# Kernel optimization log

Hardware: AMD Instinct MI355X
Metric: run time of the kernel (lower is better)

## Reference

```python
import jax, jax.numpy as jnp
import numpy as np

EPS = 1e-6
TEMPERATURE = 0.75
SINKHORN_ITERS = 7
BUCKETS = 128


def setup_inputs() -> dict:
    key = jax.random.key(0)
    k1, k2, k3, k4, k5 = jax.random.split(key, 5)
    b, h, t, dh = 2, 8, 8192, 128
    q = jax.random.normal(k1, (b, h, t, dh), dtype=jnp.float32)
    k = jax.random.normal(k2, (b, h, t, dh), dtype=jnp.float32)
    v = jax.random.normal(k3, (b, h, t, dh), dtype=jnp.float32)
    # SimpleSortNet linear: (1, heads, 2*dim_head, buckets)
    W_sort = jax.random.normal(k4, (1, h, 2 * dh, BUCKETS), dtype=jnp.float32)
    # uniform noise used to build gumbel samples (torch samples internally)
    u_gumbel = jax.random.uniform(k5, (b * h, BUCKETS, BUCKETS), dtype=jnp.float32)
    return {"q": q, "k": k, "v": v, "W_sort": W_sort, "u_gumbel": u_gumbel}


def _gumbel_sinkhorn(R, u):
    # R >= 0 (post-relu). r = (log(R+eps) + gumbel) / temperature
    g = -jnp.log(-jnp.log(u + EPS) + EPS)
    r = (jnp.log(R + EPS) + g) / TEMPERATURE
    for _ in range(SINKHORN_ITERS):
        r = r - jax.nn.logsumexp(r, axis=2, keepdims=True)
        r = r - jax.nn.logsumexp(r, axis=1, keepdims=True)
    return jnp.exp(r)


def reference(q, k, v, W_sort, u_gumbel):
    b, h, t, dh = q.shape
    dim = h * dh  # full model dim, used for the softmax scale (matches torch)
    bh = b * h
    buckets = W_sort.shape[-1]
    bsz = t // buckets

    qm = q.reshape(bh, t, dh)
    km = k.reshape(bh, t, dh)
    vm = v.reshape(bh, t, dh)

    b_q = qm.reshape(bh, buckets, bsz, dh)
    b_k = km.reshape(bh, buckets, bsz, dh)
    b_v = vm.reshape(bh, buckets, bsz, dh)

    # SimpleSortNet: per-bucket sums of q and k -> linear -> relu
    x = jnp.concatenate([b_q.sum(axis=2), b_k.sum(axis=2)], axis=-1)  # (bh, buckets, 2*dh)
    W = jnp.broadcast_to(W_sort, (b, h, 2 * dh, buckets)).reshape(bh, 2 * dh, buckets)
    R = jax.nn.relu(jnp.einsum('bue,bek->buk', x, W))  # (bh, buckets, buckets)

    R = _gumbel_sinkhorn(R, u_gumbel)

    # zero_all_but_top along dim=2 with k=1 (keep argmax entry per row)
    idx = jnp.argmax(R, axis=2, keepdims=True)  # (bh, buckets, 1)
    mask = jnp.arange(buckets)[None, None, :] == idx
    R = jnp.where(mask, R, 0.0)

    # reorder buckets: butd = sum_v R[buv] * b_k[bvtd]
    b_k_r = jnp.einsum('buv,bvtd->butd', R, b_k)
    b_v_r = jnp.einsum('buv,bvtd->butd', R, b_v)

    b_k_cat = jnp.concatenate([b_k_r, b_k], axis=2)  # (bh, buckets, 2*bsz, dh)
    b_v_cat = jnp.concatenate([b_v_r, b_v], axis=2)

    dots = jnp.einsum('buie,buje->buij', b_q, b_k_cat) * (dim ** -0.5)
    attn = jax.nn.softmax(dots, axis=-1)
    out = jnp.einsum('buij,buje->buie', attn, b_v_cat)  # (bh, buckets, bsz, dh)

    return out.reshape(b, h, t, dh)
```

## Files before the change

kernel.cpp:

```cpp
#include <hip/hip_runtime.h>
#include <hip/hip_bf16.h>

#define T_SEQ   8192
#define DH      128
#define NBH     16
#define NBUCK   128
#define BSZ     64
#define EPSF    1e-6f

#define SWZ(r) (((((r) & 7) ^ (((r) >> 3) & 7))) << 3)

typedef __attribute__((ext_vector_type(8))) __bf16 bf16x8;
typedef __attribute__((ext_vector_type(4))) float  f32x4;

static __device__ __forceinline__ unsigned short f2bf(float f) {
  __bf16 h = (__bf16)f;
  return __builtin_bit_cast(unsigned short, h);
}

__global__ __launch_bounds__(256) void k_bsum(
    const float* __restrict__ q, const float* __restrict__ k,
    float* __restrict__ x) {
  const int u = blockIdx.x, bh = blockIdx.y, which = blockIdx.z;
  const int t = threadIdx.x;
  const int c4g = t & 31;
  const int r0  = (t >> 5) << 3;
  const float* src = which ? k : q;
  const float* p = src + ((size_t)bh * T_SEQ + (size_t)u * BSZ + r0) * DH + c4g * 4;
  float4 acc = {0.f, 0.f, 0.f, 0.f};
  #pragma unroll
  for (int r = 0; r < 8; r++) {
    float4 vv = *(const float4*)(p + (size_t)r * DH);
    acc.x += vv.x; acc.y += vv.y; acc.z += vv.z; acc.w += vv.w;
  }
  __shared__ float4 xr[8][32];
  xr[t >> 5][c4g] = acc;
  __syncthreads();
  if (t < 32) {
    float4 s4 = xr[0][t];
    #pragma unroll
    for (int j = 1; j < 8; j++) {
      float4 o = xr[j][t];
      s4.x += o.x; s4.y += o.y; s4.z += o.z; s4.w += o.w;
    }
    *(float4*)(x + ((size_t)bh * NBUCK + u) * 256 + which * 128 + t * 4) = s4;
  }
}

__global__ __launch_bounds__(128) void k_sortgemm(
    const float* __restrict__ x, const float* __restrict__ W,
    const float* __restrict__ ug, float* __restrict__ rbuf) {
  const int u0 = blockIdx.x * 4, bh = blockIdx.y;
  const int v = threadIdx.x;
  __shared__ float xs[4][256];
  for (int i = v; i < 1024; i += 128)
    xs[i >> 8][i & 255] = x[((size_t)bh * NBUCK + u0 + (i >> 8)) * 256 + (i & 255)];
  __syncthreads();
  const float* Wp = W + (size_t)(bh & 7) * 256 * NBUCK + v;
  float acc0 = 0.f, acc1 = 0.f, acc2 = 0.f, acc3 = 0.f;
  #pragma unroll 16
  for (int e = 0; e < 256; e++) {
    float we = Wp[(size_t)e * NBUCK];
    acc0 += xs[0][e] * we;
    acc1 += xs[1][e] * we;
    acc2 += xs[2][e] * we;
    acc3 += xs[3][e] * we;
  }
  float accs[4] = {acc0, acc1, acc2, acc3};
  #pragma unroll
  for (int j = 0; j < 4; j++) {
    float R = fmaxf(accs[j], 0.f) + EPSF;
    float gu = ug[((size_t)bh * NBUCK + u0 + j) * NBUCK + v] + EPSF;
    float g = -logf(-logf(gu) + EPSF);
    rbuf[((size_t)bh * NBUCK + u0 + j) * NBUCK + v] = (logf(R) + g) * (1.f / 0.75f);
  }
}

__global__ __launch_bounds__(512, 1) void k_sinkhorn(
    const float* __restrict__ rbuf, int* __restrict__ idxb, float* __restrict__ sb) {
  const int bh = blockIdx.x;
  const int t  = threadIdx.x;
  const int own = t >> 2;
  const int qq  = t & 3;
  __shared__ float rl[128 * 129];
  __shared__ float ca[128], ra[128];

  const float* rb = rbuf + (size_t)bh * (NBUCK * NBUCK);
  for (int i = t; i < NBUCK * NBUCK; i += 512)
    rl[(i >> 7) * 129 + (i & 127)] = rb[i];
  if (t < 128) ca[t] = 0.f;
  __syncthreads();

  float rowv[32], colv[32];
  #pragma unroll
  for (int i4 = 0; i4 < 8; i4++) {
    float4 vv = *(const float4*)(&rl[own * 129 + qq * 32 + i4 * 4]);
    rowv[i4 * 4 + 0] = vv.x; rowv[i4 * 4 + 1] = vv.y;
    rowv[i4 * 4 + 2] = vv.z; rowv[i4 * 4 + 3] = vv.w;
  }
  #pragma unroll
  for (int i = 0; i < 32; i++) colv[i] = rl[(qq * 32 + i) * 129 + own];

  for (int iter = 0; iter < 7; iter++) {
    {
      float vals[32];
      float m = -1e30f;
      #pragma unroll
      for (int i4 = 0; i4 < 8; i4++) {
        float4 cc = *(const float4*)(&ca[qq * 32 + i4 * 4]);
        vals[i4 * 4 + 0] = rowv[i4 * 4 + 0] + cc.x;
        vals[i4 * 4 + 1] = rowv[i4 * 4 + 1] + cc.y;
        vals[i4 * 4 + 2] = rowv[i4 * 4 + 2] + cc.z;
        vals[i4 * 4 + 3] = rowv[i4 * 4 + 3] + cc.w;
      }
      #pragma unroll
      for (int i = 0; i < 32; i++) m = fmaxf(m, vals[i]);
      m = fmaxf(m, __shfl_xor(m, 1));
      m = fmaxf(m, __shfl_xor(m, 2));
      float s0 = 0.f, s1 = 0.f, s2 = 0.f, s3 = 0.f;
      #pragma unroll
      for (int i = 0; i < 8; i++) {
        s0 += __expf(vals[i * 4 + 0] - m);
        s1 += __expf(vals[i * 4 + 1] - m);
        s2 += __expf(vals[i * 4 + 2] - m);
        s3 += __expf(vals[i * 4 + 3] - m);
      }
      float ss = (s0 + s1) + (s2 + s3);
      ss += __shfl_xor(ss, 1);
      ss += __shfl_xor(ss, 2);
      if (qq == 0) ra[own] = -(m + logf(ss));
    }
    __syncthreads();
    {
      float vals[32];
      float m = -1e30f;
      #pragma unroll
      for (int i4 = 0; i4 < 8; i4++) {
        float4 rr = *(const float4*)(&ra[qq * 32 + i4 * 4]);
        vals[i4 * 4 + 0] = colv[i4 * 4 + 0] + rr.x;
        vals[i4 * 4 + 1] = colv[i4 * 4 + 1] + rr.y;
        vals[i4 * 4 + 2] = colv[i4 * 4 + 2] + rr.z;
        vals[i4 * 4 + 3] = colv[i4 * 4 + 3] + rr.w;
      }
      #pragma unroll
      for (int i = 0; i < 32; i++) m = fmaxf(m, vals[i]);
      m = fmaxf(m, __shfl_xor(m, 1));
      m = fmaxf(m, __shfl_xor(m, 2));
      float s0 = 0.f, s1 = 0.f, s2 = 0.f, s3 = 0.f;
      #pragma unroll
      for (int i = 0; i < 8; i++) {
        s0 += __expf(vals[i * 4 + 0] - m);
        s1 += __expf(vals[i * 4 + 1] - m);
        s2 += __expf(vals[i * 4 + 2] - m);
        s3 += __expf(vals[i * 4 + 3] - m);
      }
      float ss = (s0 + s1) + (s2 + s3);
      ss += __shfl_xor(ss, 1);
      ss += __shfl_xor(ss, 2);
      if (qq == 0) ca[own] = -(m + logf(ss));
    }
    __syncthreads();
  }

  {
    float best = -1e30f; int bi = qq * 32;
    #pragma unroll
    for (int i = 0; i < 32; i++) {
      float val = rowv[i] + ca[qq * 32 + i];
      if (val > best) { best = val; bi = qq * 32 + i; }
    }
    #pragma unroll
    for (int d = 1; d < 4; d <<= 1) {
      float ob = __shfl_xor(best, d);
      int   oi = __shfl_xor(bi, d);
      if (ob > best || (ob == best && oi < bi)) { best = ob; bi = oi; }
    }
    if (qq == 0) {
      idxb[bh * NBUCK + own] = bi;
      sb[bh * NBUCK + own]   = expf(rl[own * 129 + bi] + ra[own] + ca[bi]);
    }
  }
}

__global__ __launch_bounds__(256) void k_attn(
    const float* __restrict__ q, const float* __restrict__ k, const float* __restrict__ v,
    const int* __restrict__ idxb, const float* __restrict__ sb, float* __restrict__ out) {
  const int u  = blockIdx.x;
  const int bh = blockIdx.y;
  const int t  = threadIdx.x;
  const int lane = t & 63;
  const int w  = t >> 6;
  const int l15 = lane & 15;
  const int lgp = lane >> 4;

  __shared__ uint4 smem4[2048];
  unsigned short* sm = (unsigned short*)smem4;
  #define VOFF 8192

  const int   vidx = idxb[bh * NBUCK + u];
  const float sval = sb[bh * NBUCK + u];
  const size_t hb = (size_t)bh * (T_SEQ * DH);
  const float* qg = q + hb;
  const float* kg = k + hb;
  const float* vg = v + hb;

  #pragma unroll
  for (int it = 0; it < 16; it++) {
    int i = it * 256 + t;
    int row = i >> 5;
    int c4 = (i & 31) << 2;
    int grow = (row < 64) ? (vidx * BSZ + row) : (u * BSZ + (row - 64));
    float4 val = *(const float4*)(kg + (size_t)grow * DH + c4);
    ushort4 hh;
    hh.x = f2bf(val.x); hh.y = f2bf(val.y); hh.z = f2bf(val.z); hh.w = f2bf(val.w);
    *(ushort4*)(sm + (((row * 128 + c4) ^ SWZ(row)))) = hh;
  }
  bf16x8 aQ[4];
  {
    int qrow = u * BSZ + w * 16 + l15;
    const float* qp = qg + (size_t)qrow * DH + lgp * 8;
    #pragma unroll
    for (int kk = 0; kk < 4; kk++) {
      float4 v0 = *(const float4*)(qp + kk * 32);
      float4 v1 = *(const float4*)(qp + kk * 32 + 4);
      bf16x8 f;
      f[0] = (__bf16)v0.x; f[1] = (__bf16)v0.y; f[2] = (__bf16)v0.z; f[3] = (__bf16)v0.w;
      f[4] = (__bf16)v1.x; f[5] = (__bf16)v1.y; f[6] = (__bf16)v1.z; f[7] = (__bf16)v1.w;
      aQ[kk] = f;
    }
  }
  float4 vpre1[8];
  #pragma unroll
  for (int it = 0; it < 8; it++) {
    int i = it * 256 + t;
    int d0 = (i & 31) << 2;
    int j  = i >> 5;
    vpre1[it] = *(const float4*)(vg + (size_t)(vidx * BSZ + j) * DH + d0);
  }
  __syncthreads();

  f32x4 accS[8];
  __builtin_amdgcn_s_setprio(1);
  #pragma unroll
  for (int n = 0; n < 8; n++) {
    f32x4 acc = {0.f, 0.f, 0.f, 0.f};
    #pragma unroll
    for (int kk = 0; kk < 4; kk++) {
      int row = n * 16 + l15;
      int c0 = lgp * 8 + kk * 32;
      bf16x8 bK = *(const bf16x8*)(sm + ((row * 128 + c0) ^ SWZ(row)));
      acc = __builtin_amdgcn_mfma_f32_16x16x32_bf16(aQ[kk], bK, acc, 0, 0, 0);
    }
    accS[n] = acc;
  }
  __builtin_amdgcn_s_setprio(0);

  float pval[8][4];
  float lsum[4];
  #pragma unroll
  for (int r = 0; r < 4; r++) {
    float mm = -1e30f;
    #pragma unroll
    for (int n = 0; n < 8; n++) {
      float lg2 = accS[n][r] * 0.03125f * (n < 4 ? sval : 1.0f);
      pval[n][r] = lg2;
      mm = fmaxf(mm, lg2);
    }
    mm = fmaxf(mm, __shfl_xor(mm, 1));
    mm = fmaxf(mm, __shfl_xor(mm, 2));
    mm = fmaxf(mm, __shfl_xor(mm, 4));
    mm = fmaxf(mm, __shfl_xor(mm, 8));
    float ss = 0.f;
    #pragma unroll
    for (int n = 0; n < 8; n++) {
      float p = __expf(pval[n][r] - mm);
      ss += p;
      pval[n][r] = p * (n < 4 ? sval : 1.0f);
    }
    ss += __shfl_xor(ss, 1);
    ss += __shfl_xor(ss, 2);
    ss += __shfl_xor(ss, 4);
    ss += __shfl_xor(ss, 8);
    lsum[r] = ss;
  }

  __syncthreads();

  #pragma unroll
  for (int n = 0; n < 8; n++) {
    #pragma unroll
    for (int r = 0; r < 4; r++) {
      int prow = w * 16 + lgp * 4 + r;
      int pcol = n * 16 + l15;
      sm[(prow * 128 + pcol) ^ SWZ(prow)] = f2bf(pval[n][r]);
    }
  }
  #pragma unroll
  for (int it = 0; it < 8; it++) {
    int i = it * 256 + t;
    int d0 = (i & 31) << 2;
    int j  = i >> 5;
    float4 val = vpre1[it];
    sm[VOFF + (((d0 + 0) * 64 + j) ^ SWZ(d0 + 0))] = f2bf(val.x);
    sm[VOFF + (((d0 + 1) * 64 + j) ^ SWZ(d0 + 1))] = f2bf(val.y);
    sm[VOFF + (((d0 + 2) * 64 + j) ^ SWZ(d0 + 2))] = f2bf(val.z);
    sm[VOFF + (((d0 + 3) * 64 + j) ^ SWZ(d0 + 3))] = f2bf(val.w);
  }
  float4 vpre2[8];
  #pragma unroll
  for (int it = 0; it < 8; it++) {
    int i = it * 256 + t;
    int d0 = (i & 31) << 2;
    int j  = i >> 5;
    vpre2[it] = *(const float4*)(vg + (size_t)(u * BSZ + j) * DH + d0);
  }
  __syncthreads();

  bf16x8 aP[4];
  #pragma unroll
  for (int kk = 0; kk < 4; kk++) {
    int prow = w * 16 + l15;
    int c0 = lgp * 8 + kk * 32;
    aP[kk] = *(const bf16x8*)(sm + ((prow * 128 + c0) ^ SWZ(prow)));
  }

  f32x4 accO[8];
  __builtin_amdgcn_s_setprio(1);
  #pragma unroll
  for (int n = 0; n < 8; n++) {
    f32x4 acc = {0.f, 0.f, 0.f, 0.f};
    #pragma unroll
    for (int kk = 0; kk < 2; kk++) {
      int d = n * 16 + l15;
      int jj0 = lgp * 8 + kk * 32;
      bf16x8 bV = *(const bf16x8*)(sm + VOFF + ((d * 64 + jj0) ^ SWZ(d)));
      acc = __builtin_amdgcn_mfma_f32_16x16x32_bf16(aP[kk], bV, acc, 0, 0, 0);
    }
    accO[n] = acc;
  }
  __builtin_amdgcn_s_setprio(0);
  __syncthreads();

  #pragma unroll
  for (int it = 0; it < 8; it++) {
    int i = it * 256 + t;
    int d0 = (i & 31) << 2;
    int j  = i >> 5;
    float4 val = vpre2[it];
    sm[VOFF + (((d0 + 0) * 64 + j) ^ SWZ(d0 + 0))] = f2bf(val.x);
    sm[VOFF + (((d0 + 1) * 64 + j) ^ SWZ(d0 + 1))] = f2bf(val.y);
    sm[VOFF + (((d0 + 2) * 64 + j) ^ SWZ(d0 + 2))] = f2bf(val.z);
    sm[VOFF + (((d0 + 3) * 64 + j) ^ SWZ(d0 + 3))] = f2bf(val.w);
  }
  __syncthreads();

  float invl[4];
  #pragma unroll
  for (int r = 0; r < 4; r++) invl[r] = 1.0f / lsum[r];

  __builtin_amdgcn_s_setprio(1);
  #pragma unroll
  for (int n = 0; n < 8; n++) {
    f32x4 acc = accO[n];
    #pragma unroll
    for (int kk = 2; kk < 4; kk++) {
      int d = n * 16 + l15;
      int jj0 = lgp * 8 + (kk - 2) * 32;
      bf16x8 bV = *(const bf16x8*)(sm + VOFF + ((d * 64 + jj0) ^ SWZ(d)));
      acc = __builtin_amdgcn_mfma_f32_16x16x32_bf16(aP[kk], bV, acc, 0, 0, 0);
    }
    #pragma unroll
    for (int r = 0; r < 4; r++) {
      int i2 = w * 16 + lgp * 4 + r;
      int d = n * 16 + l15;
      out[((size_t)bh * T_SEQ + (size_t)u * BSZ + i2) * DH + d] = acc[r] * invl[r];
    }
  }
  __builtin_amdgcn_s_setprio(0);
}

extern "C" void kernel_launch(void* const* d_in, const int* in_sizes, int n_in,
                              void* d_out, int out_size, void* d_ws, size_t ws_size,
                              hipStream_t stream) {
  (void)in_sizes; (void)n_in; (void)out_size; (void)ws_size;
  const float* q  = (const float*)d_in[0];
  const float* k  = (const float*)d_in[1];
  const float* v  = (const float*)d_in[2];
  const float* W  = (const float*)d_in[3];
  const float* ug = (const float*)d_in[4];
  float* out = (float*)d_out;

  float* xbuf = (float*)d_ws;
  float* rbuf = xbuf + (size_t)NBH * NBUCK * 256;
  int*   idxb = (int*)(rbuf + (size_t)NBH * NBUCK * NBUCK);
  float* sb   = (float*)(idxb + NBH * NBUCK);

  k_bsum    <<<dim3(NBUCK, NBH, 2), 256, 0, stream>>>(q, k, xbuf);
  k_sortgemm<<<dim3(32, NBH),       128, 0, stream>>>(xbuf, W, ug, rbuf);
  k_sinkhorn<<<NBH,                 512, 0, stream>>>(rbuf, idxb, sb);
  k_attn    <<<dim3(NBUCK, NBH),    256, 0, stream>>>(q, k, v, idxb, sb, out);
}
```

Measured before the change: 114.0 us.

## Read K fragments directly from global and stage full V transposed in LDS

The attention kernel no longer stages K in shared memory. Each wave loads its K MFMA operand fragments straight from global memory and converts them to bf16 in registers. The LDS instead holds the full 128-row V tile transposed, filled in one pass, plus a separate P region, so the PV product runs as a single 4-step MFMA loop and several barriers and the split V staging go away. The trade-off is K rows being re-read from global/L2 by all four waves, more LDS per block, and scattered 2-byte LDS stores for the V transpose.

```diff
diff --git a/kernel.cpp b/kernel.cpp
--- a/kernel.cpp
+++ b/kernel.cpp
@@ -193,9 +193,9 @@
   const int l15 = lane & 15;
   const int lgp = lane >> 4;
 
-  __shared__ uint4 smem4[2048];
+  __shared__ uint4 smem4[3072];
   unsigned short* sm = (unsigned short*)smem4;
-  #define VOFF 8192
+  #define PB 16384
 
   const int   vidx = idxb[bh * NBUCK + u];
   const float sval = sb[bh * NBUCK + u];
@@ -207,14 +207,16 @@
   #pragma unroll
   for (int it = 0; it < 16; it++) {
     int i = it * 256 + t;
-    int row = i >> 5;
-    int c4 = (i & 31) << 2;
-    int grow = (row < 64) ? (vidx * BSZ + row) : (u * BSZ + (row - 64));
-    float4 val = *(const float4*)(kg + (size_t)grow * DH + c4);
-    ushort4 hh;
-    hh.x = f2bf(val.x); hh.y = f2bf(val.y); hh.z = f2bf(val.z); hh.w = f2bf(val.w);
-    *(ushort4*)(sm + (((row * 128 + c4) ^ SWZ(row)))) = hh;
-  }
+    int j = i & 127;
+    int d0 = (i >> 7) << 2;
+    int grow = (j < 64) ? (vidx * BSZ + j) : (u * BSZ + (j - 64));
+    float4 val = *(const float4*)(vg + (size_t)grow * DH + d0);
+    sm[(((d0 + 0) * 128 + j) ^ SWZ(d0 + 0))] = f2bf(val.x);
+    sm[(((d0 + 1) * 128 + j) ^ SWZ(d0 + 1))] = f2bf(val.y);
+    sm[(((d0 + 2) * 128 + j) ^ SWZ(d0 + 2))] = f2bf(val.z);
+    sm[(((d0 + 3) * 128 + j) ^ SWZ(d0 + 3))] = f2bf(val.w);
+  }
+
   bf16x8 aQ[4];
   {
     int qrow = u * BSZ + w * 16 + l15;
@@ -229,31 +231,26 @@
       aQ[kk] = f;
     }
   }
-  float4 vpre1[8];
-  #pragma unroll
-  for (int it = 0; it < 8; it++) {
-    int i = it * 256 + t;
-    int d0 = (i & 31) << 2;
-    int j  = i >> 5;
-    vpre1[it] = *(const float4*)(vg + (size_t)(vidx * BSZ + j) * DH + d0);
-  }
-  __syncthreads();
-
+
+  const float* kb0 = kg + (size_t)(vidx * BSZ) * DH;
+  const float* kb1 = kg + (size_t)(u    * BSZ) * DH;
   f32x4 accS[8];
-  __builtin_amdgcn_s_setprio(1);
-  #pragma unroll
+  #pragma unroll 2
   for (int n = 0; n < 8; n++) {
+    const float* kp = ((n < 4) ? (kb0 + (size_t)(n * 16 + l15) * DH)
+                               : (kb1 + (size_t)((n - 4) * 16 + l15) * DH)) + lgp * 8;
     f32x4 acc = {0.f, 0.f, 0.f, 0.f};
     #pragma unroll
     for (int kk = 0; kk < 4; kk++) {
-      int row = n * 16 + l15;
-      int c0 = lgp * 8 + kk * 32;
-      bf16x8 bK = *(const bf16x8*)(sm + ((row * 128 + c0) ^ SWZ(row)));
-      acc = __builtin_amdgcn_mfma_f32_16x16x32_bf16(aQ[kk], bK, acc, 0, 0, 0);
+      float4 a = *(const float4*)(kp + kk * 32);
+      float4 b = *(const float4*)(kp + kk * 32 + 4);
+      bf16x8 f;
+      f[0] = (__bf16)a.x; f[1] = (__bf16)a.y; f[2] = (__bf16)a.z; f[3] = (__bf16)a.w;
+      f[4] = (__bf16)b.x; f[5] = (__bf16)b.y; f[6] = (__bf16)b.z; f[7] = (__bf16)b.w;
+      acc = __builtin_amdgcn_mfma_f32_16x16x32_bf16(aQ[kk], f, acc, 0, 0, 0);
     }
     accS[n] = acc;
   }
-  __builtin_amdgcn_s_setprio(0);
 
   float pval[8][4];
   float lsum[4];
@@ -284,89 +281,38 @@
     lsum[r] = ss;
   }
 
-  __syncthreads();
-
   #pragma unroll
   for (int n = 0; n < 8; n++) {
     #pragma unroll
     for (int r = 0; r < 4; r++) {
       int prow = w * 16 + lgp * 4 + r;
       int pcol = n * 16 + l15;
-      sm[(prow * 128 + pcol) ^ SWZ(prow)] = f2bf(pval[n][r]);
-    }
-  }
-  #pragma unroll
-  for (int it = 0; it < 8; it++) {
-    int i = it * 256 + t;
-    int d0 = (i & 31) << 2;
-    int j  = i >> 5;
-    float4 val = vpre1[it];
-    sm[VOFF + (((d0 + 0) * 64 + j) ^ SWZ(d0 + 0))] = f2bf(val.x);
-    sm[VOFF + (((d0 + 1) * 64 + j) ^ SWZ(d0 + 1))] = f2bf(val.y);
-    sm[VOFF + (((d0 + 2) * 64 + j) ^ SWZ(d0 + 2))] = f2bf(val.z);
-    sm[VOFF + (((d0 + 3) * 64 + j) ^ SWZ(d0 + 3))] = f2bf(val.w);
-  }
-  float4 vpre2[8];
-  #pragma unroll
-  for (int it = 0; it < 8; it++) {
-    int i = it * 256 + t;
-    int d0 = (i & 31) << 2;
-    int j  = i >> 5;
-    vpre2[it] = *(const float4*)(vg + (size_t)(u * BSZ + j) * DH + d0);
-  }
-  __syncthreads();
-
+      sm[PB + ((prow * 128 + pcol) ^ SWZ(prow))] = f2bf(pval[n][r]);
+    }
+  }
   bf16x8 aP[4];
   #pragma unroll
   for (int kk = 0; kk < 4; kk++) {
     int prow = w * 16 + l15;
     int c0 = lgp * 8 + kk * 32;
-    aP[kk] = *(const bf16x8*)(sm + ((prow * 128 + c0) ^ SWZ(prow)));
-  }
-
-  f32x4 accO[8];
+    aP[kk] = *(const bf16x8*)(sm + PB + ((prow * 128 + c0) ^ SWZ(prow)));
+  }
+
+  __syncthreads();
+
+  float invl[4];
+  #pragma unroll
+  for (int r = 0; r < 4; r++) invl[r] = 1.0f / lsum[r];
+
   __builtin_amdgcn_s_setprio(1);
   #pragma unroll
   for (int n = 0; n < 8; n++) {
     f32x4 acc = {0.f, 0.f, 0.f, 0.f};
     #pragma unroll
-    for (int kk = 0; kk < 2; kk++) {
+    for (int kk = 0; kk < 4; kk++) {
       int d = n * 16 + l15;
       int jj0 = lgp * 8 + kk * 32;
-      bf16x8 bV = *(const bf16x8*)(sm + VOFF + ((d * 64 + jj0) ^ SWZ(d)));
-      acc = __builtin_amdgcn_mfma_f32_16x16x32_bf16(aP[kk], bV, acc, 0, 0, 0);
-    }
-    accO[n] = acc;
-  }
-  __builtin_amdgcn_s_setprio(0);
-  __syncthreads();
-
-  #pragma unroll
-  for (int it = 0; it < 8; it++) {
-    int i = it * 256 + t;
-    int d0 = (i & 31) << 2;
-    int j  = i >> 5;
-    float4 val = vpre2[it];
-    sm[VOFF + (((d0 + 0) * 64 + j) ^ SWZ(d0 + 0))] = f2bf(val.x);
-    sm[VOFF + (((d0 + 1) * 64 + j) ^ SWZ(d0 + 1))] = f2bf(val.y);
-    sm[VOFF + (((d0 + 2) * 64 + j) ^ SWZ(d0 + 2))] = f2bf(val.z);
-    sm[VOFF + (((d0 + 3) * 64 + j) ^ SWZ(d0 + 3))] = f2bf(val.w);
-  }
-  __syncthreads();
-
-  float invl[4];
-  #pragma unroll
-  for (int r = 0; r < 4; r++) invl[r] = 1.0f / lsum[r];
-
-  __builtin_amdgcn_s_setprio(1);
-  #pragma unroll
-  for (int n = 0; n < 8; n++) {
-    f32x4 acc = accO[n];
-    #pragma unroll
-    for (int kk = 2; kk < 4; kk++) {
-      int d = n * 16 + l15;
-      int jj0 = lgp * 8 + (kk - 2) * 32;
-      bf16x8 bV = *(const bf16x8*)(sm + VOFF + ((d * 64 + jj0) ^ SWZ(d)));
+      bf16x8 bV = *(const bf16x8*)(sm + ((d * 128 + jj0) ^ SWZ(d)));
       acc = __builtin_amdgcn_mfma_f32_16x16x32_bf16(aP[kk], bV, acc, 0, 0, 0);
     }
     #pragma unroll
```

After: 149.5 us. 31.2% more time.

## Stage first V block in its own LDS buffer and drop attention barriers

Applied to the files above, without the earlier changes.

The attention kernel now converts the reordered V bucket to bf16 and stores it in a dedicated shared-memory region during the initial load phase, instead of holding it in registers until after the softmax. Each wave writes its probability rows into LDS and immediately reads them back without a block barrier, because it only reads rows it wrote itself. The second V block is loaded into registers earlier and stored after the first PV MMA. Two __syncthreads are removed and the V and P swizzles are changed. In exchange, shared memory per block grows from 32 KB to 48 KB, which may lower occupancy.

```diff
diff --git a/kernel.cpp b/kernel.cpp
--- a/kernel.cpp
+++ b/kernel.cpp
@@ -8,7 +8,9 @@
 #define BSZ     64
 #define EPSF    1e-6f
 
-#define SWZ(r) (((((r) & 7) ^ (((r) >> 3) & 7))) << 3)
+#define SWZ(r)  (((((r) & 7) ^ (((r) >> 3) & 7))) << 3)
+#define VSWZ(d) ((((d) >> 2) & 7) << 3)
+#define PSWZ(r) ((((r) >> 2) & 3) << 4)
 
 typedef __attribute__((ext_vector_type(8))) __bf16 bf16x8;
 typedef __attribute__((ext_vector_type(4))) float  f32x4;
@@ -193,9 +195,10 @@
   const int l15 = lane & 15;
   const int lgp = lane >> 4;
 
-  __shared__ uint4 smem4[2048];
+  __shared__ uint4 smem4[3072];
   unsigned short* sm = (unsigned short*)smem4;
-  #define VOFF 8192
+  #define VB1 16384
+  #define VB2 8192
 
   const int   vidx = idxb[bh * NBUCK + u];
   const float sval = sb[bh * NBUCK + u];
@@ -215,6 +218,17 @@
     hh.x = f2bf(val.x); hh.y = f2bf(val.y); hh.z = f2bf(val.z); hh.w = f2bf(val.w);
     *(ushort4*)(sm + (((row * 128 + c4) ^ SWZ(row)))) = hh;
   }
+  #pragma unroll
+  for (int it = 0; it < 8; it++) {
+    int i = it * 256 + t;
+    int d0 = (i & 31) << 2;
+    int j  = i >> 5;
+    float4 val = *(const float4*)(vg + (size_t)(vidx * BSZ + j) * DH + d0);
+    sm[VB1 + (((d0 + 0) * 64 + j) ^ VSWZ(d0 + 0))] = f2bf(val.x);
+    sm[VB1 + (((d0 + 1) * 64 + j) ^ VSWZ(d0 + 1))] = f2bf(val.y);
+    sm[VB1 + (((d0 + 2) * 64 + j) ^ VSWZ(d0 + 2))] = f2bf(val.z);
+    sm[VB1 + (((d0 + 3) * 64 + j) ^ VSWZ(d0 + 3))] = f2bf(val.w);
+  }
   bf16x8 aQ[4];
   {
     int qrow = u * BSZ + w * 16 + l15;
@@ -229,14 +243,6 @@
       aQ[kk] = f;
     }
   }
-  float4 vpre1[8];
-  #pragma unroll
-  for (int it = 0; it < 8; it++) {
-    int i = it * 256 + t;
-    int d0 = (i & 31) << 2;
-    int j  = i >> 5;
-    vpre1[it] = *(const float4*)(vg + (size_t)(vidx * BSZ + j) * DH + d0);
-  }
   __syncthreads();
 
   f32x4 accS[8];
@@ -286,71 +292,59 @@
 
   __syncthreads();
 
-  #pragma unroll
-  for (int n = 0; n < 8; n++) {
-    #pragma unroll
-    for (int r = 0; r < 4; r++) {
-      int prow = w * 16 + lgp * 4 + r;
-      int pcol = n * 16 + l15;
-      sm[(prow * 128 + pcol) ^ SWZ(prow)] = f2bf(pval[n][r]);
-    }
-  }
+  ushort4 v2s[8];
   #pragma unroll
   for (int it = 0; it < 8; it++) {
     int i = it * 256 + t;
     int d0 = (i & 31) << 2;
     int j  = i >> 5;
-    float4 val = vpre1[it];
-    sm[VOFF + (((d0 + 0) * 64 + j) ^ SWZ(d0 + 0))] = f2bf(val.x);
-    sm[VOFF + (((d0 + 1) * 64 + j) ^ SWZ(d0 + 1))] = f2bf(val.y);
-    sm[VOFF + (((d0 + 2) * 64 + j) ^ SWZ(d0 + 2))] = f2bf(val.z);
-    sm[VOFF + (((d0 + 3) * 64 + j) ^ SWZ(d0 + 3))] = f2bf(val.w);
-  }
-  float4 vpre2[8];
+    float4 val = *(const float4*)(vg + (size_t)(u * BSZ + j) * DH + d0);
+    v2s[it].x = f2bf(val.x); v2s[it].y = f2bf(val.y);
+    v2s[it].z = f2bf(val.z); v2s[it].w = f2bf(val.w);
+  }
+
+  #pragma unroll
+  for (int n = 0; n < 8; n++) {
+    #pragma unroll
+    for (int r = 0; r < 4; r++) {
+      int prow = w * 16 + lgp * 4 + r;
+      int pcol = n * 16 + l15;
+      sm[(prow * 128 + pcol) ^ PSWZ(prow)] = f2bf(pval[n][r]);
+    }
+  }
+  bf16x8 aP[4];
+  #pragma unroll
+  for (int kk = 0; kk < 4; kk++) {
+    int prow = w * 16 + l15;
+    int c0 = lgp * 8 + kk * 32;
+    aP[kk] = *(const bf16x8*)(sm + ((prow * 128 + c0) ^ PSWZ(prow)));
+  }
+
+  f32x4 accO[8];
+  __builtin_amdgcn_s_setprio(1);
+  #pragma unroll
+  for (int n = 0; n < 8; n++) {
+    f32x4 acc = {0.f, 0.f, 0.f, 0.f};
+    #pragma unroll
+    for (int kk = 0; kk < 2; kk++) {
+      int d = n * 16 + l15;
+      int jj0 = lgp * 8 + kk * 32;
+      bf16x8 bV = *(const bf16x8*)(sm + VB1 + ((d * 64 + jj0) ^ VSWZ(d)));
+      acc = __builtin_amdgcn_mfma_f32_16x16x32_bf16(aP[kk], bV, acc, 0, 0, 0);
+    }
+    accO[n] = acc;
+  }
+  __builtin_amdgcn_s_setprio(0);
+
   #pragma unroll
   for (int it = 0; it < 8; it++) {
     int i = it * 256 + t;
     int d0 = (i & 31) << 2;
     int j  = i >> 5;
-    vpre2[it] = *(const float4*)(vg + (size_t)(u * BSZ + j) * DH + d0);
-  }
-  __syncthreads();
-
-  bf16x8 aP[4];
-  #pragma unroll
-  for (int kk = 0; kk < 4; kk++) {
-    int prow = w * 16 + l15;
-    int c0 = lgp * 8 + kk * 32;
-    aP[kk] = *(const bf16x8*)(sm + ((prow * 128 + c0) ^ SWZ(prow)));
-  }
-
-  f32x4 accO[8];
-  __builtin_amdgcn_s_setprio(1);
-  #pragma unroll
-  for (int n = 0; n < 8; n++) {
-    f32x4 acc = {0.f, 0.f, 0.f, 0.f};
-    #pragma unroll
-    for (int kk = 0; kk < 2; kk++) {
-      int d = n * 16 + l15;
-      int jj0 = lgp * 8 + kk * 32;
-      bf16x8 bV = *(const bf16x8*)(sm + VOFF + ((d * 64 + jj0) ^ SWZ(d)));
-      acc = __builtin_amdgcn_mfma_f32_16x16x32_bf16(aP[kk], bV, acc, 0, 0, 0);
-    }
-    accO[n] = acc;
-  }
-  __builtin_amdgcn_s_setprio(0);
-  __syncthreads();
-
-  #pragma unroll
-  for (int it = 0; it < 8; it++) {
-    int i = it * 256 + t;
-    int d0 = (i & 31) << 2;
-    int j  = i >> 5;
-    float4 val = vpre2[it];
-    sm[VOFF + (((d0 + 0) * 64 + j) ^ SWZ(d0 + 0))] = f2bf(val.x);
-    sm[VOFF + (((d0 + 1) * 64 + j) ^ SWZ(d0 + 1))] = f2bf(val.y);
-    sm[VOFF + (((d0 + 2) * 64 + j) ^ SWZ(d0 + 2))] = f2bf(val.z);
-    sm[VOFF + (((d0 + 3) * 64 + j) ^ SWZ(d0 + 3))] = f2bf(val.w);
+    sm[VB2 + (((d0 + 0) * 64 + j) ^ VSWZ(d0 + 0))] = v2s[it].x;
+    sm[VB2 + (((d0 + 1) * 64 + j) ^ VSWZ(d0 + 1))] = v2s[it].y;
+    sm[VB2 + (((d0 + 2) * 64 + j) ^ VSWZ(d0 + 2))] = v2s[it].z;
+    sm[VB2 + (((d0 + 3) * 64 + j) ^ VSWZ(d0 + 3))] = v2s[it].w;
   }
   __syncthreads();
 
@@ -366,7 +360,7 @@
     for (int kk = 2; kk < 4; kk++) {
       int d = n * 16 + l15;
       int jj0 = lgp * 8 + (kk - 2) * 32;
-      bf16x8 bV = *(const bf16x8*)(sm + VOFF + ((d * 64 + jj0) ^ SWZ(d)));
+      bf16x8 bV = *(const bf16x8*)(sm + VB2 + ((d * 64 + jj0) ^ VSWZ(d)));
       acc = __builtin_amdgcn_mfma_f32_16x16x32_bf16(aP[kk], bV, acc, 0, 0, 0);
     }
     #pragma unroll
```

Result: no change. 115.9 us (+1.7%).
